# Optimization experiments

Hardware: AMD Instinct MI355X
Metric: run time of the kernel (lower is better)

## Reference

```python
import jax, jax.numpy as jnp
import numpy as np

EMB = 1024
NH = 16
HD = EMB // NH
FF = 4 * EMB
B, T = 2, 2048
LN_EPS = 1e-5


def setup_inputs() -> dict:
    key = jax.random.key(0)
    ks = jax.random.split(key, 16)
    s = 0.02
    return {
        "x": jax.random.normal(ks[0], (B, T, EMB), jnp.float32),
        "wq": jax.random.normal(ks[1], (EMB, EMB), jnp.float32) * s,
        "bq": jnp.zeros((EMB,), jnp.float32),
        "wk": jax.random.normal(ks[2], (EMB, EMB), jnp.float32) * s,
        "bk": jnp.zeros((EMB,), jnp.float32),
        "wv": jax.random.normal(ks[3], (EMB, EMB), jnp.float32) * s,
        "bv": jnp.zeros((EMB,), jnp.float32),
        "wo": jax.random.normal(ks[4], (EMB, EMB), jnp.float32) * s,
        "bo": jnp.zeros((EMB,), jnp.float32),
        "w1": jax.random.normal(ks[5], (EMB, FF), jnp.float32) * s,
        "b1": jnp.zeros((FF,), jnp.float32),
        "w2": jax.random.normal(ks[6], (FF, EMB), jnp.float32) * s,
        "b2": jnp.zeros((EMB,), jnp.float32),
        "ln1_g": jnp.ones((EMB,), jnp.float32),
        "ln1_b": jnp.zeros((EMB,), jnp.float32),
        "ln2_g": jnp.ones((EMB,), jnp.float32),
        "ln2_b": jnp.zeros((EMB,), jnp.float32),
        "alpha_attn": jnp.float32(0.5),
        "alpha_ff": jnp.float32(0.5),
    }


def _layernorm(x, g, b):
    mu = jnp.mean(x, axis=-1, keepdims=True)
    var = jnp.var(x, axis=-1, keepdims=True)
    return (x - mu) * jax.lax.rsqrt(var + LN_EPS) * g + b


def reference(x, wq, bq, wk, bk, wv, bv, wo, bo, w1, b1, w2, b2,
              ln1_g, ln1_b, ln2_g, ln2_b, alpha_attn, alpha_ff):
    residual = x
    x_ = _layernorm(x, ln1_g, ln1_b)
    # [B,T,E] -> [B,H,T,D]
    def heads(y):
        return y.reshape(B, T, NH, HD).transpose(0, 2, 1, 3)
    q = heads(x_ @ wq + bq)
    k = heads(x_ @ wk + bk)
    v = heads(x_ @ wv + bv)
    scores = jnp.einsum("bhqd,bhkd->bhqk", q, k) / np.sqrt(HD).astype(np.float32)
    causal = jnp.tril(jnp.ones((T, T), dtype=bool))
    scores = jnp.where(causal, scores, -jnp.inf)
    attn = jax.nn.softmax(scores, axis=-1)  # dropout is identity in eval mode
    out = jnp.einsum("bhqk,bhkd->bhqd", attn, v)
    out = out.transpose(0, 2, 1, 3).reshape(B, T, EMB)
    out = out @ wo + bo
    x = residual + alpha_attn * out
    x2 = _layernorm(x, ln2_g, ln2_b)
    ff = jax.nn.gelu(x2 @ w1 + b1, approximate=False) @ w2 + b2
    return x + alpha_ff * ff
```

## Files before the change

### kernel.cpp

```cpp
#include <hip/hip_runtime.h>
#include <cmath>

#define EMB 1024
#define NH 16
#define HD 64
#define FF_DIM 4096
#define BB 2
#define TT 2048
#define NTOK (BB * TT)
#define QKVS 3072
#define SC2F 0.18033688011112042f

typedef _Float16 f16x8 __attribute__((ext_vector_type(8)));
typedef _Float16 f16x4 __attribute__((ext_vector_type(4)));
typedef float f32x4 __attribute__((ext_vector_type(4)));

__device__ __forceinline__ float gelu_fast(float x) {
    float u = x * (1.f + 0.044715f * x * x);
    float e = exp2f(u * 2.302118751f);
    return x - x / (e + 1.f);
}

template <typename TIN>
__global__ __launch_bounds__(256) void ln_kernel(const TIN* __restrict__ xin,
                                                 _Float16* __restrict__ out,
                                                 const float* __restrict__ g,
                                                 const float* __restrict__ bv) {
    int tid = threadIdx.x;
    size_t base = (size_t)blockIdx.x * EMB;
    float v[4];
#pragma unroll
    for (int i = 0; i < 4; ++i) v[i] = (float)xin[base + i * 256 + tid];
    float s = v[0] + v[1] + v[2] + v[3];
    float ss = v[0] * v[0] + v[1] * v[1] + v[2] * v[2] + v[3] * v[3];
#pragma unroll
    for (int off = 32; off > 0; off >>= 1) {
        s += __shfl_down(s, off);
        ss += __shfl_down(ss, off);
    }
    __shared__ float red[8];
    int wave = tid >> 6;
    if ((tid & 63) == 0) { red[wave] = s; red[4 + wave] = ss; }
    __syncthreads();
    s = red[0] + red[1] + red[2] + red[3];
    ss = red[4] + red[5] + red[6] + red[7];
    float mu = s * (1.0f / EMB);
    float var = ss * (1.0f / EMB) - mu * mu;
    float rstd = rsqrtf(var + 1e-5f);
#pragma unroll
    for (int i = 0; i < 4; ++i) {
        int idx = i * 256 + tid;
        float y = (v[i] - mu) * rstd * g[idx] + bv[idx];
        out[base + idx] = (_Float16)y;
    }
}

__global__ __launch_bounds__(256) void prep0_kernel(const float* __restrict__ x,
                                                    _Float16* __restrict__ xn,
                                                    const float* __restrict__ ln1_g,
                                                    const float* __restrict__ ln1_b,
                                                    const float* __restrict__ wq,
                                                    const float* __restrict__ wk,
                                                    const float* __restrict__ wv,
                                                    const float* __restrict__ wo,
                                                    const float* __restrict__ bq,
                                                    const float* __restrict__ bk,
                                                    const float* __restrict__ bv,
                                                    _Float16* __restrict__ wqkvT,
                                                    _Float16* __restrict__ woT,
                                                    float* __restrict__ qkvbias) {
    __shared__ float tile[32][33];
    int blk = blockIdx.x;
    int tid = threadIdx.x;
    if (blk >= 4108) {
        size_t base = (size_t)(blk - 4108) * EMB;
        float v[4];
#pragma unroll
        for (int i = 0; i < 4; ++i) v[i] = x[base + i * 256 + tid];
        float s = v[0] + v[1] + v[2] + v[3];
        float ss = v[0] * v[0] + v[1] * v[1] + v[2] * v[2] + v[3] * v[3];
#pragma unroll
        for (int off = 32; off > 0; off >>= 1) {
            s += __shfl_down(s, off);
            ss += __shfl_down(ss, off);
        }
        float* red = &tile[0][0];
        int wave = tid >> 6;
        if ((tid & 63) == 0) { red[wave] = s; red[4 + wave] = ss; }
        __syncthreads();
        s = red[0] + red[1] + red[2] + red[3];
        ss = red[4] + red[5] + red[6] + red[7];
        float mu = s * (1.0f / EMB);
        float var = ss * (1.0f / EMB) - mu * mu;
        float rstd = rsqrtf(var + 1e-5f);
#pragma unroll
        for (int i = 0; i < 4; ++i) {
            int idx = i * 256 + tid;
            xn[base + idx] = (_Float16)((v[i] - mu) * rstd * ln1_g[idx] + ln1_b[idx]);
        }
        return;
    }
    if (blk >= 4096) {
        int i = (blk - 4096) * 256 + tid;
        qkvbias[i] = i < 1024 ? bq[i] : (i < 2048 ? bk[i - 1024] : bv[i - 2048]);
        return;
    }
    const float* W;
    _Float16* Wt;
    int t = blk & 1023;
    int z = blk >> 10;
    if (z == 0) { W = wq; Wt = wqkvT; }
    else if (z == 1) { W = wk; Wt = wqkvT + 1024 * 1024; }
    else if (z == 2) { W = wv; Wt = wqkvT + 2 * 1024 * 1024; }
    else { W = wo; Wt = woT; }
    int bx = (t & 31) * 32, by = (t >> 5) * 32;
    int tx = tid & 31, ty = tid >> 5;
#pragma unroll
    for (int i = 0; i < 32; i += 8)
        tile[ty + i][tx] = W[(size_t)(by + ty + i) * EMB + bx + tx];
    __syncthreads();
#pragma unroll
    for (int i = 0; i < 32; i += 8)
        Wt[(size_t)(bx + ty + i) * EMB + by + tx] = (_Float16)tile[tx][ty + i];
}

__global__ __launch_bounds__(256) void prep2_kernel(const float* __restrict__ w1,
                                                    const float* __restrict__ w2,
                                                    _Float16* __restrict__ w1T,
                                                    _Float16* __restrict__ w2T) {
    int b = blockIdx.x;
    const float* W;
    _Float16* Wt;
    int K, N, t;
    if (b < 4096) { W = w1; Wt = w1T; K = 1024; N = 4096; t = b; }
    else { W = w2; Wt = w2T; K = 4096; N = 1024; t = b - 4096; }
    int ntx = N >> 5;
    int bx = (t % ntx) * 32, by = (t / ntx) * 32;
    __shared__ float tile[32][33];
    int tx = threadIdx.x & 31, ty = threadIdx.x >> 5;
#pragma unroll
    for (int i = 0; i < 32; i += 8)
        tile[ty + i][tx] = W[(size_t)(by + ty + i) * N + bx + tx];
    __syncthreads();
#pragma unroll
    for (int i = 0; i < 32; i += 8)
        Wt[(size_t)(bx + ty + i) * K + by + tx] = (_Float16)tile[tx][ty + i];
}

__global__ __launch_bounds__(256) void vT_kernel(const _Float16* __restrict__ qkv,
                                                 _Float16* __restrict__ VtG) {
    __shared__ _Float16 tile[64][72];
    int tid = threadIdx.x;
    int bh = blockIdx.y;
    int b = bh >> 4, h = bh & 15;
    int t0 = blockIdx.x * 64;
    const _Float16* src = qkv + (size_t)b * TT * QKVS + 2048 + h * HD;
    int r = tid >> 3;
    int c8 = (tid & 7) * 8;
#pragma unroll
    for (int p = 0; p < 2; ++p)
        *(f16x8*)(&tile[r + p * 32][c8]) =
            *(const f16x8*)(src + (size_t)(t0 + r + p * 32) * QKVS + c8);
    __syncthreads();
#pragma unroll
    for (int p = 0; p < 2; ++p) {
        int d = r + p * 32;
        f16x8 v;
#pragma unroll
        for (int j = 0; j < 8; ++j) v[j] = tile[c8 + j][d];
        *(f16x8*)(VtG + ((size_t)bh * HD + d) * TT + t0 + c8) = v;
    }
}

template <int MODE>
__global__ __launch_bounds__(256) void gemm_f16t(const _Float16* __restrict__ A,
                                                 const _Float16* __restrict__ Bt,
                                                 const float* __restrict__ bias,
                                                 void* __restrict__ outp,
                                                 void* __restrict__ vtg,
                                                 int M, int N, int K, int lda, int ldb) {
    __shared__ _Float16 As[128][64];
    __shared__ _Float16 Bs[128][64];
    int tid = threadIdx.x;
    int lane = tid & 63, w = tid >> 6;
    int quad = lane >> 4, l15 = lane & 15;
    int wm = (w >> 1) * 64, wn = (w & 1) * 64;
    int bM = blockIdx.y * 128, bN = blockIdx.x * 128;
    int lr = lane >> 3;
    int lcs = ((lane & 7) ^ lr) * 8;
    int sw = l15 & 7;
    f32x4 acc[4][4] = {};

    const _Float16* Abase = A + (size_t)(bM + w * 32 + lr) * lda + lcs;
    const _Float16* Bbase = Bt + (size_t)(bN + w * 32 + lr) * ldb + lcs;

    for (int kt = 0; kt < K; kt += 64) {
#pragma unroll
        for (int i = 0; i < 4; ++i) {
            __builtin_amdgcn_global_load_lds(
                (const __attribute__((address_space(1))) void*)(Abase + (size_t)(i * 8) * lda + kt),
                (__attribute__((address_space(3))) void*)(&As[w * 32 + i * 8][0]), 16, 0, 0);
            __builtin_amdgcn_global_load_lds(
                (const __attribute__((address_space(1))) void*)(Bbase + (size_t)(i * 8) * ldb + kt),
                (__attribute__((address_space(3))) void*)(&Bs[w * 32 + i * 8][0]), 16, 0, 0);
        }
        __syncthreads();
#pragma unroll
        for (int ks = 0; ks < 2; ++ks) {
            f16x8 af[4], bf[4];
#pragma unroll
            for (int i = 0; i < 4; ++i) {
                int sc = ((ks * 4 + quad) ^ sw) * 8;
                af[i] = *(const f16x8*)(&As[wm + i * 16 + l15][sc]);
                bf[i] = *(const f16x8*)(&Bs[wn + i * 16 + l15][sc]);
            }
#pragma unroll
            for (int i = 0; i < 4; ++i)
#pragma unroll
                for (int j = 0; j < 4; ++j)
                    acc[i][j] = __builtin_amdgcn_mfma_f32_16x16x32_f16(af[i], bf[j], acc[i][j], 0, 0, 0);
        }
        __syncthreads();
    }

    if (MODE == 6 && vtg != nullptr && bN >= 2048) {
        int bb = bM >> 11;
        int tbase = (bM & 2047) + wm;
#pragma unroll
        for (int i = 0; i < 4; ++i)
#pragma unroll
            for (int j = 0; j < 4; ++j) {
                int hd = bN - 2048 + wn + j * 16;
                int col = 2048 + hd + l15;
                _Float16* dst = (_Float16*)vtg +
                    (((size_t)(bb * 16 + (hd >> 6)) * 64) + (hd & 63) + l15) * TT +
                    tbase + i * 16 + quad * 4;
                f16x4 ov;
#pragma unroll
                for (int r = 0; r < 4; ++r) ov[r] = (_Float16)(acc[i][j][r] + bias[col]);
                *(f16x4*)dst = ov;
            }
        return;
    }

#pragma unroll
    for (int i = 0; i < 4; ++i)
#pragma unroll
        for (int j = 0; j < 4; ++j)
#pragma unroll
            for (int r = 0; r < 4; ++r) {
                int row = bM + wm + i * 16 + quad * 4 + r;
                int col = bN + wn + j * 16 + l15;
                size_t idx = (size_t)row * N + col;
                float vv = acc[i][j][r] + bias[col];
                if (MODE == 6) {
                    if (bN < 1024) vv *= SC2F;
                    ((_Float16*)outp)[idx] = (_Float16)vv;
                } else {
                    ((_Float16*)outp)[idx] = (_Float16)gelu_fast(vv);
                }
            }
}

template <int MODE>
__global__ __launch_bounds__(256) void gemm64(const _Float16* __restrict__ A,
                                              const _Float16* __restrict__ Bt,
                                              const float* __restrict__ bias,
                                              void* __restrict__ outp,
                                              const void* __restrict__ residp,
                                              const float* __restrict__ alphap,
                                              int M, int N, int K, int lda, int ldb) {
    __shared__ _Float16 As[128][64];
    __shared__ _Float16 Bs[64][64];
    int tid = threadIdx.x;
    int lane = tid & 63, w = tid >> 6;
    int quad = lane >> 4, l15 = lane & 15;
    int wm = w * 32;
    int bM = blockIdx.y * 128, bN = blockIdx.x * 64;
    int lr = lane >> 3;
    int lcs = ((lane & 7) ^ lr) * 8;
    int sw = l15 & 7;
    int kz = (MODE == 7) ? blockIdx.z * K : 0;
    f32x4 acc[2][4] = {};

    const _Float16* Abase = A + (size_t)(bM + w * 32 + lr) * lda + kz + lcs;
    const _Float16* Bbase = Bt + (size_t)(bN + w * 16 + lr) * ldb + kz + lcs;

    for (int kt = 0; kt < K; kt += 64) {
#pragma unroll
        for (int i = 0; i < 4; ++i)
            __builtin_amdgcn_global_load_lds(
                (const __attribute__((address_space(1))) void*)(Abase + (size_t)(i * 8) * lda + kt),
                (__attribute__((address_space(3))) void*)(&As[w * 32 + i * 8][0]), 16, 0, 0);
#pragma unroll
        for (int i = 0; i < 2; ++i)
            __builtin_amdgcn_global_load_lds(
                (const __attribute__((address_space(1))) void*)(Bbase + (size_t)(i * 8) * ldb + kt),
                (__attribute__((address_space(3))) void*)(&Bs[w * 16 + i * 8][0]), 16, 0, 0);
        __syncthreads();
#pragma unroll
        for (int ks = 0; ks < 2; ++ks) {
            int sc = ((ks * 4 + quad) ^ sw) * 8;
            f16x8 af[2], bf[4];
#pragma unroll
            for (int i = 0; i < 2; ++i)
                af[i] = *(const f16x8*)(&As[wm + i * 16 + l15][sc]);
#pragma unroll
            for (int j = 0; j < 4; ++j)
                bf[j] = *(const f16x8*)(&Bs[j * 16 + l15][sc]);
#pragma unroll
            for (int i = 0; i < 2; ++i)
#pragma unroll
                for (int j = 0; j < 4; ++j)
                    acc[i][j] = __builtin_amdgcn_mfma_f32_16x16x32_f16(af[i], bf[j], acc[i][j], 0, 0, 0);
        }
        __syncthreads();
    }

    float alpha = 0.f;
    if (MODE == 2 || MODE == 5) alpha = alphap[0];
    _Float16* pout = nullptr;
    if (MODE == 7) pout = blockIdx.z ? (_Float16*)(void*)residp : (_Float16*)outp;
#pragma unroll
    for (int i = 0; i < 2; ++i)
#pragma unroll
        for (int j = 0; j < 4; ++j)
#pragma unroll
            for (int r = 0; r < 4; ++r) {
                int row = bM + wm + i * 16 + quad * 4 + r;
                int col = bN + j * 16 + l15;
                size_t idx = (size_t)row * N + col;
                if (MODE == 7) {
                    pout[idx] = (_Float16)acc[i][j][r];
                } else if (MODE == 4) {
                    ((float*)outp)[idx] = acc[i][j][r];
                } else if (MODE == 2) {
                    float vv = acc[i][j][r] + bias[col];
                    float rsd = ((const float*)residp)[idx];
                    ((_Float16*)outp)[idx] = (_Float16)(rsd + alpha * vv);
                } else {
                    float vv = acc[i][j][r] + bias[col];
                    float prev = ((float*)outp)[idx];
                    float rsd = (float)((const _Float16*)residp)[idx];
                    ((float*)outp)[idx] = rsd + alpha * (prev + vv);
                }
            }
}

__global__ __launch_bounds__(256) void ff2_reduce_kernel(const _Float16* __restrict__ p0,
                                                         const _Float16* __restrict__ p1,
                                                         const _Float16* __restrict__ xmid,
                                                         const float* __restrict__ b2,
                                                         const float* __restrict__ alphap,
                                                         float* __restrict__ out) {
    int i = (blockIdx.x * 256 + threadIdx.x) * 8;
    float alpha = alphap[0];
    f16x8 a = *(const f16x8*)(p0 + i);
    f16x8 b = *(const f16x8*)(p1 + i);
    f16x8 xm = *(const f16x8*)(xmid + i);
    int col = i & 1023;
#pragma unroll
    for (int k = 0; k < 8; ++k)
        out[i + k] = (float)xm[k] + alpha * ((float)a[k] + (float)b[k] + b2[col + k]);
}

#define QT 64
#define NEG_BIG (-1e30f)
__global__ __launch_bounds__(512) void attn_mfma_kernel(const _Float16* __restrict__ qkv,
                                                        const _Float16* __restrict__ VtG,
                                                        _Float16* __restrict__ O) {
    __shared__ _Float16 Ks[64][72];
    __shared__ _Float16 Vt[64][72];
    __shared__ _Float16 Ps[8][16][68];
    int tid = threadIdx.x;
    int lane = tid & 63, w = tid >> 6;
    int quad = lane >> 4, l15 = lane & 15;
    int bh = blockIdx.x;
    int b = bh >> 4, h = bh & 15;
    int y = blockIdx.y;
    int seg = w >> 2, ws = w & 3;
    int qt = seg ? y : (31 - y);
    int q0 = qt * QT;
    int ntw = qt + 1;
    int ntmax = 32 - y;
    const _Float16* Qh = qkv + (size_t)b * TT * QKVS + h * HD;
    const _Float16* Kh = Qh + 1024;
    const _Float16* Vrows = VtG + (size_t)bh * HD * TT;

    int m0 = q0 + ws * 16;
    f16x8 aq0 = *(const f16x8*)(Qh + (size_t)(m0 + l15) * QKVS + quad * 8);
    f16x8 aq1 = *(const f16x8*)(Qh + (size_t)(m0 + l15) * QKVS + 32 + quad * 8);

    f32x4 Oacc[4] = {};
    float lrow[4] = {0.f, 0.f, 0.f, 0.f};

    int rr = tid >> 3;
    int c8 = (tid & 7) * 8;
    const _Float16* Kp = Kh + (size_t)rr * QKVS + c8;
    const _Float16* Vp = Vrows + (size_t)rr * TT + c8;

    f16x8 kreg = *(const f16x8*)(Kp);
    f16x8 vreg = *(const f16x8*)(Vp);

    for (int t = 0; t < ntmax; ++t) {
        int t0 = t * 64;
        __syncthreads();
        *(f16x8*)(&Ks[rr][c8]) = kreg;
        *(f16x8*)(&Vt[rr][c8]) = vreg;
        __syncthreads();
        if (t + 1 < ntmax) {
            kreg = *(const f16x8*)(Kp + (size_t)(t0 + 64) * QKVS);
            vreg = *(const f16x8*)(Vp + t0 + 64);
        }
        if (t >= ntw) continue;

        f32x4 Sacc[4] = {};
        __builtin_amdgcn_s_setprio(1);
#pragma unroll
        for (int nc = 0; nc < 4; ++nc) {
            f16x8 bk0 = *(const f16x8*)(&Ks[nc * 16 + l15][quad * 8]);
            f16x8 bk1 = *(const f16x8*)(&Ks[nc * 16 + l15][32 + quad * 8]);
            Sacc[nc] = __builtin_amdgcn_mfma_f32_16x16x32_f16(aq0, bk0, Sacc[nc], 0, 0, 0);
            Sacc[nc] = __builtin_amdgcn_mfma_f32_16x16x32_f16(aq1, bk1, Sacc[nc], 0, 0, 0);
        }
        __builtin_amdgcn_s_setprio(0);

        if (t0 == q0) {
#pragma unroll
            for (int nc = 0; nc < 4; ++nc) {
                int key = t0 + nc * 16 + l15;
#pragma unroll
                for (int i = 0; i < 4; ++i)
                    if (key > m0 + quad * 4 + i) Sacc[nc][i] = NEG_BIG;
            }
        }

#pragma unroll
        for (int nc = 0; nc < 4; ++nc)
#pragma unroll
            for (int i = 0; i < 4; ++i) {
                float p = exp2f(Sacc[nc][i]);
                lrow[i] += p;
                Ps[w][quad * 4 + i][nc * 16 + l15] = (_Float16)p;
            }
        __asm__ __volatile__("s_waitcnt lgkmcnt(0)" ::: "memory");

        f16x8 ap0 = *(const f16x8*)(&Ps[w][l15][quad * 8]);
        f16x8 ap1 = *(const f16x8*)(&Ps[w][l15][32 + quad * 8]);
        __builtin_amdgcn_s_setprio(1);
#pragma unroll
        for (int nc = 0; nc < 4; ++nc) {
            int d = nc * 16 + l15;
            f16x8 bv0 = *(const f16x8*)(&Vt[d][quad * 8]);
            f16x8 bv1 = *(const f16x8*)(&Vt[d][32 + quad * 8]);
            Oacc[nc] = __builtin_amdgcn_mfma_f32_16x16x32_f16(ap0, bv0, Oacc[nc], 0, 0, 0);
            Oacc[nc] = __builtin_amdgcn_mfma_f32_16x16x32_f16(ap1, bv1, Oacc[nc], 0, 0, 0);
        }
        __builtin_amdgcn_s_setprio(0);
    }

#pragma unroll
    for (int off = 1; off < 16; off <<= 1)
#pragma unroll
        for (int i = 0; i < 4; ++i) lrow[i] += __shfl_xor(lrow[i], off);
#pragma unroll
    for (int i = 0; i < 4; ++i) lrow[i] = 1.0f / lrow[i];
    _Float16* Oh = O + (size_t)b * TT * EMB + h * HD;
#pragma unroll
    for (int nc = 0; nc < 4; ++nc)
#pragma unroll
        for (int i = 0; i < 4; ++i) {
            int row = m0 + quad * 4 + i;
            Oh[(size_t)row * EMB + nc * 16 + l15] = (_Float16)(Oacc[nc][i] * lrow[i]);
        }
}

extern "C" void kernel_launch(void* const* d_in, const int* in_sizes, int n_in,
                              void* d_out, int out_size, void* d_ws, size_t ws_size,
                              hipStream_t stream) {
    const float* x = (const float*)d_in[0];
    const float* wq = (const float*)d_in[1];
    const float* bq = (const float*)d_in[2];
    const float* wk = (const float*)d_in[3];
    const float* bk = (const float*)d_in[4];
    const float* wv = (const float*)d_in[5];
    const float* bv = (const float*)d_in[6];
    const float* wo = (const float*)d_in[7];
    const float* bo = (const float*)d_in[8];
    const float* w1 = (const float*)d_in[9];
    const float* b1 = (const float*)d_in[10];
    const float* w2 = (const float*)d_in[11];
    const float* b2 = (const float*)d_in[12];
    const float* ln1_g = (const float*)d_in[13];
    const float* ln1_b = (const float*)d_in[14];
    const float* ln2_g = (const float*)d_in[15];
    const float* ln2_b = (const float*)d_in[16];
    const float* alpha_attn = (const float*)d_in[17];
    const float* alpha_ff = (const float*)d_in[18];

    const size_t SL = (size_t)8 * 1024 * 1024;
    char* ws = (char*)d_ws;
    _Float16* xn = (_Float16*)(ws);
    _Float16* qkv = (_Float16*)(ws + SL);
    _Float16* wqkvT = (_Float16*)(ws + 4 * SL);
    float* qkvbias = (float*)(ws + 4 * SL + 6 * 1024 * 1024);
    _Float16* attnout = (_Float16*)(ws);
    _Float16* xmid = (_Float16*)(ws + SL);
    _Float16* x2 = (_Float16*)(ws + 2 * SL);
    _Float16* w1T = (_Float16*)(ws);
    _Float16* w2T = (_Float16*)(ws + 3 * SL);
    _Float16* ff1 = (_Float16*)(ws + 4 * SL);
    bool bigws = ws_size >= (size_t)64 * 1024 * 1024;
    _Float16* VtG = bigws ? (_Float16*)(ws + 5 * SL) : (_Float16*)(ws + 4 * SL);
    _Float16* woT = bigws ? (_Float16*)(ws + 6 * SL) : (_Float16*)(ws + 5 * SL);
    _Float16* part0 = (_Float16*)(ws);
    _Float16* part1 = (_Float16*)(ws + 2 * SL);

    prep0_kernel<<<8204, 256, 0, stream>>>(x, xn, ln1_g, ln1_b, wq, wk, wv, wo,
                                           bq, bk, bv, wqkvT, woT, qkvbias);

    gemm_f16t<6><<<dim3(QKVS / 128, NTOK / 128), 256, 0, stream>>>(
        xn, wqkvT, qkvbias, qkv, bigws ? (void*)VtG : nullptr, NTOK, QKVS, EMB, EMB, EMB);
    if (!bigws)
        vT_kernel<<<dim3(TT / 64, BB * NH), 256, 0, stream>>>(qkv, VtG);

    attn_mfma_kernel<<<dim3(BB * NH, TT / QT / 2), 512, 0, stream>>>(qkv, VtG, attnout);

    gemm64<2><<<dim3(EMB / 64, NTOK / 128), 256, 0, stream>>>(
        attnout, woT, bo, xmid, x, alpha_attn, NTOK, EMB, EMB, EMB, EMB);

    ln_kernel<_Float16><<<NTOK, 256, 0, stream>>>(xmid, x2, ln2_g, ln2_b);

    prep2_kernel<<<8192, 256, 0, stream>>>(w1, w2, w1T, w2T);

    if (bigws) {
        gemm_f16t<1><<<dim3(FF_DIM / 128, NTOK / 128), 256, 0, stream>>>(
            x2, w1T, b1, ff1, nullptr, NTOK, FF_DIM, EMB, EMB, EMB);
        gemm64<7><<<dim3(EMB / 64, NTOK / 128, 2), 256, 0, stream>>>(
            ff1, w2T, nullptr, part0, part1, nullptr, NTOK, EMB, 2048, FF_DIM, FF_DIM);
        ff2_reduce_kernel<<<NTOK * EMB / 8 / 256, 256, 0, stream>>>(
            part0, part1, xmid, b2, alpha_ff, (float*)d_out);
    } else {
        const int NC = 2048;
        for (int hh = 0; hh < 2; ++hh) {
            const _Float16* w1Th = w1T + (size_t)hh * NC * EMB;
            const _Float16* w2Th = w2T + (size_t)hh * NC;
            gemm_f16t<1><<<dim3(NC / 128, NTOK / 128), 256, 0, stream>>>(
                x2, w1Th, b1 + hh * NC, ff1, nullptr, NTOK, NC, EMB, EMB, EMB);
            if (hh == 0)
                gemm64<4><<<dim3(EMB / 64, NTOK / 128), 256, 0, stream>>>(
                    ff1, w2Th, nullptr, d_out, nullptr, nullptr, NTOK, EMB, NC, NC, FF_DIM);
            else
                gemm64<5><<<dim3(EMB / 64, NTOK / 128), 256, 0, stream>>>(
                    ff1, w2Th, b2, d_out, xmid, alpha_ff, NTOK, EMB, NC, NC, FF_DIM);
        }
    }
}
```

Baseline: 375.8 us.

## Add 256x256-tile pipelined GEMM for QKV and FF1 projections

Introduces a new gemm256 kernel with 512 threads, 256x256 output tiles, double-buffered LDS filled by direct global-to-LDS loads, XOR-swizzled reads, interleaved staging and MFMA quarters with setprio, and an XCD-aware block remap. It replaces the 128x128 gemm_f16t for the QKV projection (including the fused V-transpose epilogue) and the FF1 GELU projection when the workspace is large. The aim is more data reuse per tile and overlap of loads with matrix math. In exchange it uses much more LDS and registers per block and launches far fewer blocks, which may leave some compute units idle.

```diff
diff --git a/kernel.cpp b/kernel.cpp
--- a/kernel.cpp
+++ b/kernel.cpp
@@ -254,6 +254,143 @@
                 size_t idx = (size_t)row * N + col;
                 float vv = acc[i][j][r] + bias[col];
                 if (MODE == 6) {
+                    if (bN < 1024) vv *= SC2F;
+                    ((_Float16*)outp)[idx] = (_Float16)vv;
+                } else {
+                    ((_Float16*)outp)[idx] = (_Float16)gelu_fast(vv);
+                }
+            }
+}
+
+#define STAGE_PAIR(OB, TN, I)                                                            \
+    {                                                                                    \
+        size_t ko = (size_t)(TN) * 64;                                                   \
+        __builtin_amdgcn_global_load_lds(                                                \
+            (const __attribute__((address_space(1))) void*)(Ab + (size_t)((I) * 8) * lda + ko), \
+            (__attribute__((address_space(3))) void*)(&As[OB][w * 32 + (I) * 8][0]), 16, 0, 0); \
+        __builtin_amdgcn_global_load_lds(                                                \
+            (const __attribute__((address_space(1))) void*)(Bb + (size_t)((I) * 8) * ldb + ko), \
+            (__attribute__((address_space(3))) void*)(&Bs[OB][w * 32 + (I) * 8][0]), 16, 0, 0); \
+    }
+#define RD_A(CB, I, KS) (*(const f16x8*)(&As[CB][wr * 128 + (I) * 16 + l15][(((KS)*4 + quad) ^ sw) * 8]))
+#define RD_B(CB, J, KS) (*(const f16x8*)(&Bs[CB][wc * 64 + (J) * 16 + l15][(((KS)*4 + quad) ^ sw) * 8]))
+#define MMQ(I0, J0)                                                                      \
+    __builtin_amdgcn_s_setprio(1);                                                       \
+    _Pragma("unroll") for (int ks = 0; ks < 2; ++ks) {                                   \
+        _Pragma("unroll") for (int ii = 0; ii < 4; ++ii) {                               \
+            _Pragma("unroll") for (int jj = 0; jj < 2; ++jj)                             \
+                acc[(I0) + ii][(J0) + jj] = __builtin_amdgcn_mfma_f32_16x16x32_f16(      \
+                    af[ii][ks], bf[(J0) + jj][ks], acc[(I0) + ii][(J0) + jj], 0, 0, 0);  \
+        }                                                                                \
+    }                                                                                    \
+    __builtin_amdgcn_s_setprio(0);
+#define KTILE(CB, OB, TN)                                                                \
+    {                                                                                    \
+                                                              \
+        STAGE_PAIR(OB, TN, 0);                                                           \
+        asm volatile("s_waitcnt vmcnt(2)" ::: "memory");                                 \
+        __builtin_amdgcn_s_barrier();                                                    \
+        _Pragma("unroll") for (int i = 0; i < 4; ++i) {                                  \
+            af[i][0] = RD_A(CB, i, 0);                                                   \
+            af[i][1] = RD_A(CB, i, 1);                                                   \
+        }                                                                                \
+        bf[0][0] = RD_B(CB, 0, 0); bf[0][1] = RD_B(CB, 0, 1);                            \
+        bf[1][0] = RD_B(CB, 1, 0); bf[1][1] = RD_B(CB, 1, 1);                            \
+        MMQ(0, 0);                                                                       \
+        __builtin_amdgcn_s_barrier();                                                    \
+                                                                            \
+        bf[2][0] = RD_B(CB, 2, 0); bf[2][1] = RD_B(CB, 2, 1);                            \
+        bf[3][0] = RD_B(CB, 3, 0); bf[3][1] = RD_B(CB, 3, 1);                            \
+        STAGE_PAIR(OB, TN, 1);                                                           \
+        __builtin_amdgcn_s_barrier();                                                    \
+        MMQ(0, 2);                                                                       \
+        __builtin_amdgcn_s_barrier();                                                    \
+                                                                            \
+        _Pragma("unroll") for (int i = 0; i < 4; ++i) {                                  \
+            af[i][0] = RD_A(CB, 4 + i, 0);                                               \
+            af[i][1] = RD_A(CB, 4 + i, 1);                                               \
+        }                                                                                \
+        STAGE_PAIR(OB, TN, 2);                                                           \
+        __builtin_amdgcn_s_barrier();                                                    \
+        MMQ(4, 0);                                                                       \
+        __builtin_amdgcn_s_barrier();                                                    \
+                                                                            \
+        STAGE_PAIR(OB, TN, 3);                                                           \
+        __builtin_amdgcn_s_barrier();                                                    \
+        MMQ(4, 2);                                                                       \
+        __builtin_amdgcn_s_barrier();                                                    \
+    }
+
+template <int MODE>
+__global__ __launch_bounds__(512, 2) void gemm256(const _Float16* __restrict__ A,
+                                                  const _Float16* __restrict__ Bt,
+                                                  const float* __restrict__ bias,
+                                                  void* __restrict__ outp,
+                                                  void* __restrict__ vtg,
+                                                  int M, int N, int K, int lda, int ldb) {
+    __shared__ _Float16 As[2][256][64];
+    __shared__ _Float16 Bs[2][256][64];
+    int tid = threadIdx.x;
+    int lane = tid & 63, w = tid >> 6;
+    int quad = lane >> 4, l15 = lane & 15;
+    int wr = w >> 2, wc = w & 3;
+    int gx = gridDim.x;
+    int nwg = gx * gridDim.y;
+    int bid = blockIdx.y * gx + blockIdx.x;
+    int cpx = nwg >> 3;
+    int sbid = (bid & 7) * cpx + (bid >> 3);
+    int bN = (sbid % gx) * 256;
+    int bM = (sbid / gx) * 256;
+    int lr = lane >> 3;
+    int lcs = ((lane & 7) ^ lr) * 8;
+    int sw = l15 & 7;
+    f32x4 acc[8][4] = {};
+    f16x8 af[4][2], bf[4][2];
+
+    const _Float16* Ab = A + (size_t)(bM + w * 32 + lr) * lda + lcs;
+    const _Float16* Bb = Bt + (size_t)(bN + w * 32 + lr) * ldb + lcs;
+    const int NT = K >> 6;
+
+#pragma unroll
+    for (int i = 0; i < 4; ++i) STAGE_PAIR(0, 0, i);
+
+    for (int it = 0; it < NT; it += 2) {
+        int tn1 = it + 1;
+        int tn2 = (it + 2 < NT) ? it + 2 : 0;
+        KTILE(0, 1, tn1);
+        KTILE(1, 0, tn2);
+    }
+
+    if (MODE == 1 && vtg != nullptr && bN >= 2048) {
+        int bb = bM >> 11;
+#pragma unroll
+        for (int i = 0; i < 8; ++i)
+#pragma unroll
+            for (int j = 0; j < 4; ++j) {
+                int hd = bN - 2048 + wc * 64 + j * 16;
+                int col = 2048 + hd + l15;
+                int tb = (bM & 2047) + wr * 128 + i * 16 + quad * 4;
+                _Float16* dst = (_Float16*)vtg +
+                    (((size_t)(bb * 16 + (hd >> 6)) * 64) + (hd & 63) + l15) * TT + tb;
+                f16x4 ov;
+#pragma unroll
+                for (int r = 0; r < 4; ++r) ov[r] = (_Float16)(acc[i][j][r] + bias[col]);
+                *(f16x4*)dst = ov;
+            }
+        return;
+    }
+
+#pragma unroll
+    for (int i = 0; i < 8; ++i)
+#pragma unroll
+        for (int j = 0; j < 4; ++j)
+#pragma unroll
+            for (int r = 0; r < 4; ++r) {
+                int row = bM + wr * 128 + i * 16 + quad * 4 + r;
+                int col = bN + wc * 64 + j * 16 + l15;
+                size_t idx = (size_t)row * N + col;
+                float vv = acc[i][j][r] + bias[col];
+                if (MODE == 1) {
                     if (bN < 1024) vv *= SC2F;
                     ((_Float16*)outp)[idx] = (_Float16)vv;
                 } else {
@@ -519,10 +656,14 @@
     prep0_kernel<<<8204, 256, 0, stream>>>(x, xn, ln1_g, ln1_b, wq, wk, wv, wo,
                                            bq, bk, bv, wqkvT, woT, qkvbias);
 
-    gemm_f16t<6><<<dim3(QKVS / 128, NTOK / 128), 256, 0, stream>>>(
-        xn, wqkvT, qkvbias, qkv, bigws ? (void*)VtG : nullptr, NTOK, QKVS, EMB, EMB, EMB);
-    if (!bigws)
+    if (bigws) {
+        gemm256<1><<<dim3(QKVS / 256, NTOK / 256), 512, 0, stream>>>(
+            xn, wqkvT, qkvbias, qkv, (void*)VtG, NTOK, QKVS, EMB, EMB, EMB);
+    } else {
+        gemm_f16t<6><<<dim3(QKVS / 128, NTOK / 128), 256, 0, stream>>>(
+            xn, wqkvT, qkvbias, qkv, nullptr, NTOK, QKVS, EMB, EMB, EMB);
         vT_kernel<<<dim3(TT / 64, BB * NH), 256, 0, stream>>>(qkv, VtG);
+    }
 
     attn_mfma_kernel<<<dim3(BB * NH, TT / QT / 2), 512, 0, stream>>>(qkv, VtG, attnout);
 
@@ -534,7 +675,7 @@
     prep2_kernel<<<8192, 256, 0, stream>>>(w1, w2, w1T, w2T);
 
     if (bigws) {
-        gemm_f16t<1><<<dim3(FF_DIM / 128, NTOK / 128), 256, 0, stream>>>(
+        gemm256<0><<<dim3(FF_DIM / 256, NTOK / 256), 512, 0, stream>>>(
             x2, w1T, b1, ff1, nullptr, NTOK, FF_DIM, EMB, EMB, EMB);
         gemm64<7><<<dim3(EMB / 64, NTOK / 128, 2), 256, 0, stream>>>(
             ff1, w2T, nullptr, part0, part1, nullptr, NTOK, EMB, 2048, FF_DIM, FF_DIM);
```

New measurement: 366.3 us. -2.5%, faster.
